# Optimization experiments

Measured on AMD Instinct MI355X. Metric: run time of the kernel, lower is better.

Reference implementation:

```python
import jax, jax.numpy as jnp
import numpy as np

EMBED_DIM = 1024
HEADS = 16
D_HEAD = EMBED_DIM // HEADS
B, S = 4, 2048


def setup_inputs() -> dict:
    key = jax.random.key(0)
    ks = jax.random.split(key, 7)
    scale = 1.0 / np.sqrt(EMBED_DIM)
    inp = {
        "key": jax.random.normal(ks[0], (B, S, EMBED_DIM), jnp.float32),
        "query": jax.random.normal(ks[1], (B, S, EMBED_DIM), jnp.float32),
        "value": jax.random.normal(ks[2], (B, S, EMBED_DIM), jnp.float32),
        # causal boolean mask, broadcastable to [B, H, S, S]
        "mask": jnp.tril(jnp.ones((S, S), dtype=bool))[None, None, :, :] * jnp.ones((B, 1, 1, 1), dtype=bool),
        # nn.Linear weights, stored torch-style as [out_features, in_features]
        "Wq": jax.random.normal(ks[3], (EMBED_DIM, EMBED_DIM), jnp.float32) * scale,
        "Wk": jax.random.normal(ks[4], (EMBED_DIM, EMBED_DIM), jnp.float32) * scale,
        "Wv": jax.random.normal(ks[5], (EMBED_DIM, EMBED_DIM), jnp.float32) * scale,
        "Wo": jax.random.normal(ks[6], (EMBED_DIM, EMBED_DIM), jnp.float32) * scale,
    }
    return inp


def reference(key, query, value, mask, Wq, Wk, Wv, Wo):
    # projections (nn.Linear, bias=False): x @ W.T
    q = query @ Wq.T                                    # [B,S,E]
    k = key @ Wk.T
    v = value @ Wv.T
    # split heads -> [B,H,S,d]
    def split(x):
        return x.reshape(B, S, HEADS, D_HEAD).transpose(0, 2, 1, 3)
    q, k, v = split(q), split(k), split(v)
    # scaled dot-product scores [B,H,S,S]
    scores = jnp.einsum("bhqd,bhkd->bhqk", q, k) / np.sqrt(D_HEAD).astype(np.float32)
    scores = jnp.where(mask, scores, jnp.float32(-1e9))
    attn = jax.nn.softmax(scores, axis=-1)
    # attention output, merge heads
    out = jnp.einsum("bhqk,bhkd->bhqd", attn, v)        # [B,H,S,d]
    out = out.transpose(0, 2, 1, 3).reshape(B, S, EMBED_DIM)
    return out @ Wo.T
```

## Files before the change

kernel.cpp:

```cpp
#include <hip/hip_runtime.h>

#define SEQ 2048
#define EMBED 1024
#define DHEAD 64

typedef _Float16 h8 __attribute__((ext_vector_type(8)));
typedef _Float16 h4 __attribute__((ext_vector_type(4)));
typedef float f4 __attribute__((ext_vector_type(4)));
typedef unsigned int u32;

__device__ __forceinline__ void gload_lds16(const void* g, void* l) {
    __builtin_amdgcn_global_load_lds(
        (const __attribute__((address_space(1))) u32*)g,
        (__attribute__((address_space(3))) u32*)l, 16, 0, 0);
}

__global__ __launch_bounds__(256) void cvt_f16(
    const float* __restrict__ q, const float* __restrict__ k, const float* __restrict__ v,
    const float* __restrict__ wq, const float* __restrict__ wk, const float* __restrict__ wv,
    const float* __restrict__ wo,
    _Float16* __restrict__ q16, _Float16* __restrict__ k16, _Float16* __restrict__ v16,
    _Float16* __restrict__ wq16, _Float16* __restrict__ wk16, _Float16* __restrict__ wv16,
    _Float16* __restrict__ wo16)
{
    int bid = blockIdx.x;
    const float* src;
    _Float16* dst;
    float scale = 1.0f;
    size_t base;
    if (bid < 24576) {
        int seg = bid >> 13;
        base = (size_t)(bid & 8191) * 1024 + threadIdx.x * 4;
        src = seg == 0 ? q : seg == 1 ? k : v;
        dst = seg == 0 ? q16 : seg == 1 ? k16 : v16;
    } else {
        int wb = bid - 24576;
        int seg = wb >> 10;
        base = (size_t)(wb & 1023) * 1024 + threadIdx.x * 4;
        src = seg == 0 ? wq : seg == 1 ? wk : seg == 2 ? wv : wo;
        dst = seg == 0 ? wq16 : seg == 1 ? wk16 : seg == 2 ? wv16 : wo16;
        if (seg == 0) scale = 0.18033688011112042f;
    }
    float4 x = *(const float4*)(src + base);
    h4 y = { (_Float16)(x.x * scale), (_Float16)(x.y * scale),
             (_Float16)(x.z * scale), (_Float16)(x.w * scale) };
    *(h4*)(dst + base) = y;
}

__device__ __forceinline__ void gemm_core(const _Float16* __restrict__ A, const _Float16* __restrict__ W,
                                          int m0, int n0, int tid,
                                          _Float16* As, _Float16* Bs, f4 acc[4][4])
{
    const int lane = tid & 63, wave = tid >> 6;
    const int t16 = lane & 15, quad = lane >> 4;
    const int wm = (wave >> 1) * 64, wn = (wave & 1) * 64;
    const int wb = wave * 64;
    const int u0 = tid, u1 = tid + 256;
    const int r0 = u0 >> 2, c0 = u0 & 3;
    const int r1 = u1 >> 2, c1 = u1 & 3;
    const _Float16* ga0 = A + (size_t)(m0 + r0) * 1024 + c0 * 8;
    const _Float16* ga1 = A + (size_t)(m0 + r1) * 1024 + c1 * 8;
    const _Float16* gb0 = W + (size_t)(n0 + r0) * 1024 + c0 * 8;
    const _Float16* gb1 = W + (size_t)(n0 + r1) * 1024 + c1 * 8;
    _Float16* la0 = As + wb * 8;
    _Float16* la1 = As + (256 + wb) * 8;
    _Float16* lb0 = Bs + wb * 8;
    _Float16* lb1 = Bs + (256 + wb) * 8;

    for (int k0 = 0; k0 < 1024; k0 += 32) {
        __syncthreads();
        gload_lds16(ga0 + k0, la0);
        gload_lds16(ga1 + k0, la1);
        gload_lds16(gb0 + k0, lb0);
        gload_lds16(gb1 + k0, lb1);
        __syncthreads();
        h8 af[4], bf[4];
#pragma unroll
        for (int i = 0; i < 4; ++i)
            af[i] = *(const h8*)(As + (wm + i * 16 + t16) * 32 + quad * 8);
#pragma unroll
        for (int j = 0; j < 4; ++j)
            bf[j] = *(const h8*)(Bs + (wn + j * 16 + t16) * 32 + quad * 8);
#pragma unroll
        for (int i = 0; i < 4; ++i)
#pragma unroll
            for (int j = 0; j < 4; ++j)
                acc[i][j] = __builtin_amdgcn_mfma_f32_16x16x32_f16(af[i], bf[j], acc[i][j], 0, 0, 0);
    }
}

__global__ __launch_bounds__(256) void proj_qkv(
    const _Float16* __restrict__ q16, const _Float16* __restrict__ k16, const _Float16* __restrict__ v16,
    const _Float16* __restrict__ Wq, const _Float16* __restrict__ Wk, const _Float16* __restrict__ Wv,
    _Float16* __restrict__ Qh, _Float16* __restrict__ Kh, _Float16* __restrict__ Vt)
{
    __shared__ _Float16 As[4096], Bs[4096];
    const int tid = threadIdx.x;
    const int z = blockIdx.z;
    const _Float16 *A, *W;
    int m0, n0;
    if (z == 2) { A = Wv; W = v16; m0 = blockIdx.y * 128; n0 = blockIdx.x * 128; }
    else if (z == 0) { A = q16; W = Wq; m0 = blockIdx.x * 128; n0 = blockIdx.y * 128; }
    else { A = k16; W = Wk; m0 = blockIdx.x * 128; n0 = blockIdx.y * 128; }

    f4 acc[4][4];
    const f4 z4 = {0.f, 0.f, 0.f, 0.f};
#pragma unroll
    for (int i = 0; i < 4; ++i)
#pragma unroll
        for (int j = 0; j < 4; ++j) acc[i][j] = z4;

    gemm_core(A, W, m0, n0, tid, As, Bs, acc);

    const int lane = tid & 63, wave = tid >> 6;
    const int t16 = lane & 15, quad = lane >> 4;
    const int wm = (wave >> 1) * 64, wn = (wave & 1) * 64;
#pragma unroll
    for (int i = 0; i < 4; ++i)
#pragma unroll
        for (int j = 0; j < 4; ++j)
#pragma unroll
            for (int reg = 0; reg < 4; ++reg) {
                int gm = m0 + wm + i * 16 + quad * 4 + reg;
                int gn = n0 + wn + j * 16 + t16;
                float vv = acc[i][j][reg];
                if (z < 2) {
                    int b = gm >> 11, s = gm & 2047, h = gn >> 6, dd = gn & 63;
                    _Float16* dst = (z == 0) ? Qh : Kh;
                    dst[(((size_t)(b * 16 + h) * SEQ) + s) * DHEAD + dd] = (_Float16)vv;
                } else {
                    int h = gm >> 6, dd = gm & 63, b = gn >> 11, s = gn & 2047;
                    Vt[(((size_t)(b * 16 + h) * DHEAD) + dd) * SEQ + s] = (_Float16)vv;
                }
            }
}

__global__ __launch_bounds__(256) void attn3(
    const _Float16* __restrict__ Qh, const _Float16* __restrict__ Kh,
    const _Float16* __restrict__ Vt, _Float16* __restrict__ Ob)
{
    __shared__ _Float16 Kbuf[2][8][512];
    __shared__ _Float16 Vbuf[2][8][512];
    __shared__ _Float16 Pex[4][2][2][512];

    const int tid = threadIdx.x;
    const int lane = tid & 63, wave = tid >> 6;
    const int t16 = lane & 15, quad = lane >> 4;
    const int bh = blockIdx.x;
    const int b = bh >> 4, h = bh & 15;
    const int qb = (gridDim.y - 1) - blockIdx.y;
    const int q0 = qb * 128;
    const int nqt = qb * 2 + 2;

    const _Float16* Qp = Qh + (size_t)bh * SEQ * DHEAD;
    const _Float16* Kp = Kh + (size_t)bh * SEQ * DHEAD;
    const _Float16* Vp = Vt + (size_t)bh * DHEAD * SEQ;

    const int qlo[2] = { q0 + wave * 32, q0 + wave * 32 + 16 };
    const int last0 = (qlo[0] + 15) >> 6;
    const int last1 = (qlo[1] + 15) >> 6;

    h8 qf[2][2];
#pragma unroll
    for (int qb2 = 0; qb2 < 2; ++qb2)
#pragma unroll
        for (int kc = 0; kc < 2; ++kc)
            qf[qb2][kc] = *(const h8*)(Qp + (size_t)(qlo[qb2] + t16) * 64 + kc * 32 + quad * 8);

    const _Float16* Kl = Kp + t16 * 64 + quad * 8;
    const _Float16* Vl = Vp + t16 * 2048 + quad * 8;

#define STAGE(jt_, bufi)                                                                  \
    do {                                                                                  \
        if (wave < 2) {                                                                   \
            _Pragma("unroll")                                                             \
            for (int i_ = 0; i_ < 4; ++i_) {                                              \
                int g_ = wave * 4 + i_;                                                   \
                gload_lds16(Kl + (jt_) * 4096 + (g_ >> 1) * 1024 + (g_ & 1) * 32,         \
                            &Kbuf[bufi][g_][0]);                                          \
            }                                                                             \
        } else {                                                                          \
            _Pragma("unroll")                                                             \
            for (int i_ = 0; i_ < 4; ++i_) {                                              \
                int g_ = (wave - 2) * 4 + i_;                                             \
                gload_lds16(Vl + (g_ >> 1) * 32768 + (jt_) * 64 + (g_ & 1) * 32,          \
                            &Vbuf[bufi][g_][0]);                                          \
            }                                                                             \
        }                                                                                 \
    } while (0)

    STAGE(0, 0);
    __syncthreads();

    float mv[2] = {-1e30f, -1e30f};
    float lv[2] = {0.f, 0.f};
    f4 o_acc[2][4];
    const f4 z4 = {0.f, 0.f, 0.f, 0.f};
#pragma unroll
    for (int qb2 = 0; qb2 < 2; ++qb2)
#pragma unroll
        for (int dt = 0; dt < 4; ++dt) o_acc[qb2][dt] = z4;

    for (int jt = 0; jt < nqt; ++jt) {
        const int buf = jt & 1;
        if (jt + 1 < nqt) STAGE(jt + 1, buf ^ 1);

        if (jt <= last1) {
            f4 s0[4], s1[4];
#pragma unroll
            for (int j4 = 0; j4 < 4; ++j4) {
                h8 kfa = *(const h8*)(&Kbuf[buf][j4 * 2 + 0][lane * 8]);
                h8 kfb = *(const h8*)(&Kbuf[buf][j4 * 2 + 1][lane * 8]);
                s1[j4] = __builtin_amdgcn_mfma_f32_16x16x32_f16(kfa, qf[1][0], z4, 0, 0, 0);
                s1[j4] = __builtin_amdgcn_mfma_f32_16x16x32_f16(kfb, qf[1][1], s1[j4], 0, 0, 0);
                s0[j4] = __builtin_amdgcn_mfma_f32_16x16x32_f16(kfa, qf[0][0], z4, 0, 0, 0);
                s0[j4] = __builtin_amdgcn_mfma_f32_16x16x32_f16(kfb, qf[0][1], s0[j4], 0, 0, 0);
            }

            auto softmax_store = [&](f4* s, int qb2) {
                const int myq = qlo[qb2] + t16;
                if ((jt << 6) + 63 > myq - t16 + 15 || true) {  }
                if ((jt << 6) + 63 > qlo[qb2]) {
#pragma unroll
                    for (int j4 = 0; j4 < 4; ++j4)
#pragma unroll
                        for (int reg = 0; reg < 4; ++reg) {
                            int kk = (jt << 6) + j4 * 16 + quad * 4 + reg;
                            if (kk > myq) s[j4][reg] = -1e30f;
                        }
                }
                float mr = s[0][0];
#pragma unroll
                for (int j4 = 0; j4 < 4; ++j4)
#pragma unroll
                    for (int reg = 0; reg < 4; ++reg) mr = fmaxf(mr, s[j4][reg]);
                mr = fmaxf(mr, __shfl_xor(mr, 16, 64));
                mr = fmaxf(mr, __shfl_xor(mr, 32, 64));
                float mn = fmaxf(mv[qb2], mr);
                float al = __builtin_amdgcn_exp2f(mv[qb2] - mn);
                mv[qb2] = mn;
                float rs = 0.f;
#pragma unroll
                for (int j4 = 0; j4 < 4; ++j4)
#pragma unroll
                    for (int reg = 0; reg < 4; ++reg) {
                        float p = __builtin_amdgcn_exp2f(s[j4][reg] - mn);
                        s[j4][reg] = p;
                        rs += p;
                    }
                rs += __shfl_xor(rs, 16, 64);
                rs += __shfl_xor(rs, 32, 64);
                lv[qb2] = lv[qb2] * al + rs;
#pragma unroll
                for (int dt = 0; dt < 4; ++dt)
#pragma unroll
                    for (int reg = 0; reg < 4; ++reg) o_acc[qb2][dt][reg] *= al;
#pragma unroll
                for (int j4 = 0; j4 < 4; ++j4) {
                    int Lt = (((j4 & 1) * 2 + (quad >> 1)) << 4) + t16;
                    h4 ph = { (_Float16)s[j4][0], (_Float16)s[j4][1],
                              (_Float16)s[j4][2], (_Float16)s[j4][3] };
                    *(h4*)(&Pex[wave][qb2][j4 >> 1][Lt * 8 + (quad & 1) * 4]) = ph;
                }
            };

            if (jt <= last0) {
                softmax_store(s0, 0);
                softmax_store(s1, 1);
                h8 pb0a = *(const h8*)(&Pex[wave][0][0][lane * 8]);
                h8 pb0b = *(const h8*)(&Pex[wave][0][1][lane * 8]);
                h8 pb1a = *(const h8*)(&Pex[wave][1][0][lane * 8]);
                h8 pb1b = *(const h8*)(&Pex[wave][1][1][lane * 8]);
#pragma unroll
                for (int dt = 0; dt < 4; ++dt) {
                    h8 ava = *(const h8*)(&Vbuf[buf][dt * 2 + 0][lane * 8]);
                    h8 avb = *(const h8*)(&Vbuf[buf][dt * 2 + 1][lane * 8]);
                    o_acc[0][dt] = __builtin_amdgcn_mfma_f32_16x16x32_f16(ava, pb0a, o_acc[0][dt], 0, 0, 0);
                    o_acc[0][dt] = __builtin_amdgcn_mfma_f32_16x16x32_f16(avb, pb0b, o_acc[0][dt], 0, 0, 0);
                    o_acc[1][dt] = __builtin_amdgcn_mfma_f32_16x16x32_f16(ava, pb1a, o_acc[1][dt], 0, 0, 0);
                    o_acc[1][dt] = __builtin_amdgcn_mfma_f32_16x16x32_f16(avb, pb1b, o_acc[1][dt], 0, 0, 0);
                }
            } else {
                softmax_store(s1, 1);
                h8 pb1a = *(const h8*)(&Pex[wave][1][0][lane * 8]);
                h8 pb1b = *(const h8*)(&Pex[wave][1][1][lane * 8]);
#pragma unroll
                for (int dt = 0; dt < 4; ++dt) {
                    h8 ava = *(const h8*)(&Vbuf[buf][dt * 2 + 0][lane * 8]);
                    h8 avb = *(const h8*)(&Vbuf[buf][dt * 2 + 1][lane * 8]);
                    o_acc[1][dt] = __builtin_amdgcn_mfma_f32_16x16x32_f16(ava, pb1a, o_acc[1][dt], 0, 0, 0);
                    o_acc[1][dt] = __builtin_amdgcn_mfma_f32_16x16x32_f16(avb, pb1b, o_acc[1][dt], 0, 0, 0);
                }
            }
        }
        __syncthreads();
    }

#pragma unroll
    for (int qb2 = 0; qb2 < 2; ++qb2) {
        float inv = __builtin_amdgcn_rcpf(lv[qb2]);
        _Float16* ep = &Pex[wave][qb2][0][0];
#pragma unroll
        for (int dt = 0; dt < 4; ++dt) {
            h4 ov = { (_Float16)(o_acc[qb2][dt][0] * inv), (_Float16)(o_acc[qb2][dt][1] * inv),
                      (_Float16)(o_acc[qb2][dt][2] * inv), (_Float16)(o_acc[qb2][dt][3] * inv) };
            *(h4*)(ep + t16 * 64 + dt * 16 + quad * 4) = ov;
        }
        h8 r0 = *(const h8*)(ep + t16 * 64 + quad * 8);
        h8 r1 = *(const h8*)(ep + t16 * 64 + 32 + quad * 8);
        int s = qlo[qb2] + t16;
        _Float16* og = Ob + ((size_t)(b * SEQ + s)) * EMBED + h * DHEAD;
        *(h8*)(og + quad * 8) = r0;
        *(h8*)(og + 32 + quad * 8) = r1;
    }
#undef STAGE
}

__global__ __launch_bounds__(256) void proj_out(
    const _Float16* __restrict__ A, const _Float16* __restrict__ Wo, float* __restrict__ out)
{
    __shared__ _Float16 As[4096], Bs[4096];
    const int tid = threadIdx.x;
    const int m0 = blockIdx.x * 128, n0 = blockIdx.y * 128;
    f4 acc[4][4];
    const f4 z4 = {0.f, 0.f, 0.f, 0.f};
#pragma unroll
    for (int i = 0; i < 4; ++i)
#pragma unroll
        for (int j = 0; j < 4; ++j) acc[i][j] = z4;

    gemm_core(A, Wo, m0, n0, tid, As, Bs, acc);

    const int lane = tid & 63, wave = tid >> 6;
    const int t16 = lane & 15, quad = lane >> 4;
    const int wm = (wave >> 1) * 64, wn = (wave & 1) * 64;
#pragma unroll
    for (int i = 0; i < 4; ++i)
#pragma unroll
        for (int j = 0; j < 4; ++j)
#pragma unroll
            for (int reg = 0; reg < 4; ++reg) {
                int gm = m0 + wm + i * 16 + quad * 4 + reg;
                int gn = n0 + wn + j * 16 + t16;
                out[(size_t)gm * EMBED + gn] = acc[i][j][reg];
            }
}

extern "C" void kernel_launch(void* const* d_in, const int* in_sizes, int n_in,
                              void* d_out, int out_size, void* d_ws, size_t ws_size,
                              hipStream_t stream) {
    const float* key   = (const float*)d_in[0];
    const float* query = (const float*)d_in[1];
    const float* value = (const float*)d_in[2];
    const float* Wq = (const float*)d_in[4];
    const float* Wk = (const float*)d_in[5];
    const float* Wv = (const float*)d_in[6];
    const float* Wo = (const float*)d_in[7];

    char* ws = (char*)d_ws;
    _Float16* v16  = (_Float16*)(ws);
    _Float16* Wq16 = (_Float16*)(ws + (16u << 20));
    _Float16* Wk16 = (_Float16*)(ws + (18u << 20));
    _Float16* Wv16 = (_Float16*)(ws + (20u << 20));
    _Float16* Wo16 = (_Float16*)(ws + (22u << 20));
    _Float16* Qh   = (_Float16*)(ws + (24u << 20));
    _Float16* Kh   = (_Float16*)(ws + (40u << 20));
    _Float16* Vt   = (_Float16*)(ws + (56u << 20));
    _Float16* Ob   = v16;
    _Float16* q16 = (_Float16*)d_out;
    _Float16* k16 = (_Float16*)d_out + 8388608;

    dim3 blk(256);
    cvt_f16<<<dim3(28672), blk, 0, stream>>>(query, key, value, Wq, Wk, Wv, Wo,
                                             q16, k16, v16, Wq16, Wk16, Wv16, Wo16);
    proj_qkv<<<dim3(64, 8, 3), blk, 0, stream>>>(q16, k16, v16, Wq16, Wk16, Wv16, Qh, Kh, Vt);
    attn3<<<dim3(64, 16), blk, 0, stream>>>(Qh, Kh, Vt, Ob);
    proj_out<<<dim3(64, 8), blk, 0, stream>>>(Ob, Wo16, (float*)d_out);
}
```

Measured before the change: 338.8 us.

## Use 128-key single-buffered attention tiles and widen fp16 conversion to 8 elements

```diff
diff --git a/kernel.cpp b/kernel.cpp
--- a/kernel.cpp
+++ b/kernel.cpp
@@ -28,23 +28,26 @@
     _Float16* dst;
     float scale = 1.0f;
     size_t base;
-    if (bid < 24576) {
-        int seg = bid >> 13;
-        base = (size_t)(bid & 8191) * 1024 + threadIdx.x * 4;
+    if (bid < 12288) {
+        int seg = bid >> 12;
+        base = (size_t)(bid & 4095) * 2048 + threadIdx.x * 8;
         src = seg == 0 ? q : seg == 1 ? k : v;
         dst = seg == 0 ? q16 : seg == 1 ? k16 : v16;
     } else {
-        int wb = bid - 24576;
-        int seg = wb >> 10;
-        base = (size_t)(wb & 1023) * 1024 + threadIdx.x * 4;
+        int wb = bid - 12288;
+        int seg = wb >> 9;
+        base = (size_t)(wb & 511) * 2048 + threadIdx.x * 8;
         src = seg == 0 ? wq : seg == 1 ? wk : seg == 2 ? wv : wo;
         dst = seg == 0 ? wq16 : seg == 1 ? wk16 : seg == 2 ? wv16 : wo16;
         if (seg == 0) scale = 0.18033688011112042f;
     }
-    float4 x = *(const float4*)(src + base);
-    h4 y = { (_Float16)(x.x * scale), (_Float16)(x.y * scale),
-             (_Float16)(x.z * scale), (_Float16)(x.w * scale) };
-    *(h4*)(dst + base) = y;
+    float4 x0 = *(const float4*)(src + base);
+    float4 x1 = *(const float4*)(src + base + 4);
+    h8 y = { (_Float16)(x0.x * scale), (_Float16)(x0.y * scale),
+             (_Float16)(x0.z * scale), (_Float16)(x0.w * scale),
+             (_Float16)(x1.x * scale), (_Float16)(x1.y * scale),
+             (_Float16)(x1.z * scale), (_Float16)(x1.w * scale) };
+    *(h8*)(dst + base) = y;
 }
 
 __device__ __forceinline__ void gemm_core(const _Float16* __restrict__ A, const _Float16* __restrict__ W,
@@ -135,12 +138,12 @@
             }
 }
 
-__global__ __launch_bounds__(256) void attn3(
+__global__ __launch_bounds__(256) void attn4(
     const _Float16* __restrict__ Qh, const _Float16* __restrict__ Kh,
     const _Float16* __restrict__ Vt, _Float16* __restrict__ Ob)
 {
-    __shared__ _Float16 Kbuf[2][8][512];
-    __shared__ _Float16 Vbuf[2][8][512];
+    __shared__ _Float16 Kbuf[16][512];
+    __shared__ _Float16 Vbuf[16][512];
     __shared__ _Float16 Pex[4][2][2][512];
 
     const int tid = threadIdx.x;
@@ -150,7 +153,7 @@
     const int b = bh >> 4, h = bh & 15;
     const int qb = (gridDim.y - 1) - blockIdx.y;
     const int q0 = qb * 128;
-    const int nqt = qb * 2 + 2;
+    const int njt = qb + 1;
 
     const _Float16* Qp = Qh + (size_t)bh * SEQ * DHEAD;
     const _Float16* Kp = Kh + (size_t)bh * SEQ * DHEAD;
@@ -169,28 +172,6 @@
 
     const _Float16* Kl = Kp + t16 * 64 + quad * 8;
     const _Float16* Vl = Vp + t16 * 2048 + quad * 8;
-
-#define STAGE(jt_, bufi)                                                                  \
-    do {                                                                                  \
-        if (wave < 2) {                                                                   \
-            _Pragma("unroll")                                                             \
-            for (int i_ = 0; i_ < 4; ++i_) {                                              \
-                int g_ = wave * 4 + i_;                                                   \
-                gload_lds16(Kl + (jt_) * 4096 + (g_ >> 1) * 1024 + (g_ & 1) * 32,         \
-                            &Kbuf[bufi][g_][0]);                                          \
-            }                                                                             \
-        } else {                                                                          \
-            _Pragma("unroll")                                                             \
-            for (int i_ = 0; i_ < 4; ++i_) {                                              \
-                int g_ = (wave - 2) * 4 + i_;                                             \
-                gload_lds16(Vl + (g_ >> 1) * 32768 + (jt_) * 64 + (g_ & 1) * 32,          \
-                            &Vbuf[bufi][g_][0]);                                          \
-            }                                                                             \
-        }                                                                                 \
-    } while (0)
-
-    STAGE(0, 0);
-    __syncthreads();
 
     float mv[2] = {-1e30f, -1e30f};
     float lv[2] = {0.f, 0.f};
@@ -201,31 +182,52 @@
 #pragma unroll
         for (int dt = 0; dt < 4; ++dt) o_acc[qb2][dt] = z4;
 
-    for (int jt = 0; jt < nqt; ++jt) {
-        const int buf = jt & 1;
-        if (jt + 1 < nqt) STAGE(jt + 1, buf ^ 1);
-
-        if (jt <= last1) {
+    for (int jt = 0; jt < njt; ++jt) {
+        __syncthreads();
+        if (wave < 2) {
+#pragma unroll
+            for (int i_ = 0; i_ < 8; ++i_) {
+                int g_ = wave * 8 + i_;
+                gload_lds16(Kl + (size_t)jt * 8192 + (g_ >> 1) * 1024 + (g_ & 1) * 32,
+                            &Kbuf[g_][0]);
+            }
+        } else {
+#pragma unroll
+            for (int i_ = 0; i_ < 8; ++i_) {
+                int g_ = (wave - 2) * 8 + i_;
+                gload_lds16(Vl + (size_t)(g_ >> 2) * 32768 + jt * 128 + (g_ & 3) * 32,
+                            &Vbuf[g_][0]);
+            }
+        }
+        __syncthreads();
+
+#pragma unroll
+        for (int half = 0; half < 2; ++half) {
+            const int ht = jt * 2 + half;
+            if (ht > last1) continue;
+
             f4 s0[4], s1[4];
+            const bool act0 = (ht <= last0);
 #pragma unroll
             for (int j4 = 0; j4 < 4; ++j4) {
-                h8 kfa = *(const h8*)(&Kbuf[buf][j4 * 2 + 0][lane * 8]);
-                h8 kfb = *(const h8*)(&Kbuf[buf][j4 * 2 + 1][lane * 8]);
+                h8 kfa = *(const h8*)(&Kbuf[(half * 4 + j4) * 2 + 0][lane * 8]);
+                h8 kfb = *(const h8*)(&Kbuf[(half * 4 + j4) * 2 + 1][lane * 8]);
                 s1[j4] = __builtin_amdgcn_mfma_f32_16x16x32_f16(kfa, qf[1][0], z4, 0, 0, 0);
                 s1[j4] = __builtin_amdgcn_mfma_f32_16x16x32_f16(kfb, qf[1][1], s1[j4], 0, 0, 0);
-                s0[j4] = __builtin_amdgcn_mfma_f32_16x16x32_f16(kfa, qf[0][0], z4, 0, 0, 0);
-                s0[j4] = __builtin_amdgcn_mfma_f32_16x16x32_f16(kfb, qf[0][1], s0[j4], 0, 0, 0);
+                if (act0) {
+                    s0[j4] = __builtin_amdgcn_mfma_f32_16x16x32_f16(kfa, qf[0][0], z4, 0, 0, 0);
+                    s0[j4] = __builtin_amdgcn_mfma_f32_16x16x32_f16(kfb, qf[0][1], s0[j4], 0, 0, 0);
+                }
             }
 
             auto softmax_store = [&](f4* s, int qb2) {
                 const int myq = qlo[qb2] + t16;
-                if ((jt << 6) + 63 > myq - t16 + 15 || true) {  }
-                if ((jt << 6) + 63 > qlo[qb2]) {
+                if (ht == ((qlo[qb2] + 15) >> 6)) {
 #pragma unroll
                     for (int j4 = 0; j4 < 4; ++j4)
 #pragma unroll
                         for (int reg = 0; reg < 4; ++reg) {
-                            int kk = (jt << 6) + j4 * 16 + quad * 4 + reg;
+                            int kk = ht * 64 + j4 * 16 + quad * 4 + reg;
                             if (kk > myq) s[j4][reg] = -1e30f;
                         }
                 }
@@ -264,36 +266,23 @@
                 }
             };
 
-            if (jt <= last0) {
-                softmax_store(s0, 0);
-                softmax_store(s1, 1);
-                h8 pb0a = *(const h8*)(&Pex[wave][0][0][lane * 8]);
-                h8 pb0b = *(const h8*)(&Pex[wave][0][1][lane * 8]);
-                h8 pb1a = *(const h8*)(&Pex[wave][1][0][lane * 8]);
-                h8 pb1b = *(const h8*)(&Pex[wave][1][1][lane * 8]);
-#pragma unroll
-                for (int dt = 0; dt < 4; ++dt) {
-                    h8 ava = *(const h8*)(&Vbuf[buf][dt * 2 + 0][lane * 8]);
-                    h8 avb = *(const h8*)(&Vbuf[buf][dt * 2 + 1][lane * 8]);
-                    o_acc[0][dt] = __builtin_amdgcn_mfma_f32_16x16x32_f16(ava, pb0a, o_acc[0][dt], 0, 0, 0);
-                    o_acc[0][dt] = __builtin_amdgcn_mfma_f32_16x16x32_f16(avb, pb0b, o_acc[0][dt], 0, 0, 0);
-                    o_acc[1][dt] = __builtin_amdgcn_mfma_f32_16x16x32_f16(ava, pb1a, o_acc[1][dt], 0, 0, 0);
-                    o_acc[1][dt] = __builtin_amdgcn_mfma_f32_16x16x32_f16(avb, pb1b, o_acc[1][dt], 0, 0, 0);
-                }
-            } else {
-                softmax_store(s1, 1);
-                h8 pb1a = *(const h8*)(&Pex[wave][1][0][lane * 8]);
-                h8 pb1b = *(const h8*)(&Pex[wave][1][1][lane * 8]);
-#pragma unroll
-                for (int dt = 0; dt < 4; ++dt) {
-                    h8 ava = *(const h8*)(&Vbuf[buf][dt * 2 + 0][lane * 8]);
-                    h8 avb = *(const h8*)(&Vbuf[buf][dt * 2 + 1][lane * 8]);
-                    o_acc[1][dt] = __builtin_amdgcn_mfma_f32_16x16x32_f16(ava, pb1a, o_acc[1][dt], 0, 0, 0);
-                    o_acc[1][dt] = __builtin_amdgcn_mfma_f32_16x16x32_f16(avb, pb1b, o_acc[1][dt], 0, 0, 0);
+            if (act0) softmax_store(s0, 0);
+            softmax_store(s1, 1);
+
+#pragma unroll
+            for (int dt = 0; dt < 4; ++dt) {
+#pragma unroll
+                for (int kc2 = 0; kc2 < 2; ++kc2) {
+                    h8 vf = *(const h8*)(&Vbuf[dt * 4 + half * 2 + kc2][lane * 8]);
+                    if (act0) {
+                        h8 pb0 = *(const h8*)(&Pex[wave][0][kc2][lane * 8]);
+                        o_acc[0][dt] = __builtin_amdgcn_mfma_f32_16x16x32_f16(vf, pb0, o_acc[0][dt], 0, 0, 0);
+                    }
+                    h8 pb1 = *(const h8*)(&Pex[wave][1][kc2][lane * 8]);
+                    o_acc[1][dt] = __builtin_amdgcn_mfma_f32_16x16x32_f16(vf, pb1, o_acc[1][dt], 0, 0, 0);
                 }
             }
         }
-        __syncthreads();
     }
 
 #pragma unroll
@@ -313,7 +302,6 @@
         *(h8*)(og + quad * 8) = r0;
         *(h8*)(og + 32 + quad * 8) = r1;
     }
-#undef STAGE
 }
 
 __global__ __launch_bounds__(256) void proj_out(
@@ -371,9 +359,9 @@
     _Float16* k16 = (_Float16*)d_out + 8388608;
 
     dim3 blk(256);
-    cvt_f16<<<dim3(28672), blk, 0, stream>>>(query, key, value, Wq, Wk, Wv, Wo,
+    cvt_f16<<<dim3(14336), blk, 0, stream>>>(query, key, value, Wq, Wk, Wv, Wo,
                                              q16, k16, v16, Wq16, Wk16, Wv16, Wo16);
     proj_qkv<<<dim3(64, 8, 3), blk, 0, stream>>>(q16, k16, v16, Wq16, Wk16, Wv16, Qh, Kh, Vt);
-    attn3<<<dim3(64, 16), blk, 0, stream>>>(Qh, Kh, Vt, Ob);
+    attn4<<<dim3(64, 16), blk, 0, stream>>>(Qh, Kh, Vt, Ob);
     proj_out<<<dim3(64, 8), blk, 0, stream>>>(Ob, Wo16, (float*)d_out);
 }
```

After: 356.9 us. 5.4% more time.
